# Optimization experiments

Hardware: AMD Instinct MI355X
Metric: run time of the kernel (lower is better)

## Reference

```python
import jax, jax.numpy as jnp
import numpy as np

N_NODES = 50000
N_EDGES = 800000
IN_DIM, HID_DIM, LAT_DIM = 64, 64, 32


def _glorot(key, fan_in, fan_out):
    s = jnp.sqrt(6.0 / (fan_in + fan_out))
    return jax.random.uniform(key, (fan_in, fan_out), jnp.float32, -s, s)


def setup_inputs() -> dict:
    key = jax.random.key(0)
    ks = jax.random.split(key, 8)
    x = jax.random.normal(ks[0], (N_NODES, IN_DIM), jnp.float32)
    edge_index = jax.random.randint(ks[1], (2, N_EDGES), 0, N_NODES, jnp.int64)
    W1 = _glorot(ks[2], IN_DIM, HID_DIM)
    b1 = jnp.zeros((HID_DIM,), jnp.float32)
    W2 = _glorot(ks[3], HID_DIM, HID_DIM)
    b2 = jnp.zeros((HID_DIM,), jnp.float32)
    W3 = _glorot(ks[4], HID_DIM, LAT_DIM)
    b3 = jnp.zeros((LAT_DIM,), jnp.float32)
    return {"x": x, "edge_index": edge_index, "W1": W1, "b1": b1,
            "W2": W2, "b2": b2, "W3": W3, "b3": b3}


def _self_loop_edges(edge_index, n):
    loop = jnp.arange(n, dtype=edge_index.dtype)
    src = jnp.concatenate([edge_index[0], loop])
    dst = jnp.concatenate([edge_index[1], loop])
    return src, dst


def _gcn_norm(src, dst, n):
    # deg over A + I (unit edge weights), computed on target column (PyG default)
    deg = jax.ops.segment_sum(jnp.ones_like(dst, dtype=jnp.float32), dst, num_segments=n)
    dinv = jnp.where(deg > 0, jax.lax.rsqrt(deg), 0.0)
    return dinv[src] * dinv[dst]  # [E+N]


def _gcn_conv(x, src, dst, norm, W, b, n):
    h = x @ W                         # [N, out] small GEMM first, as in PyG
    msg = h[src] * norm[:, None]      # gather + scale, [E+N, out]
    out = jax.ops.segment_sum(msg, dst, num_segments=n)  # scatter-add
    return out + b


def reference(x, edge_index, W1, b1, W2, b2, W3, b3):
    n = x.shape[0]
    src, dst = _self_loop_edges(edge_index, n)
    norm = _gcn_norm(src, dst, n)
    h = jnp.tanh(_gcn_conv(x, src, dst, norm, W1, b1, n))
    h = jnp.tanh(_gcn_conv(h, src, dst, norm, W2, b2, n))
    z = _gcn_conv(h, src, dst, norm, W3, b3, n)
    return z
```

## Files before the change

kernel.cpp:

```cpp
#include <hip/hip_runtime.h>
#include <hip/hip_bf16.h>


#define IN_DIM 64
#define HID_DIM 64
#define LAT_DIM 32
#define BCAP 5120


__global__ __launch_bounds__(256) void bin_kernel(const int* __restrict__ src,
                                                  const int* __restrict__ dst,
                                                  int* __restrict__ bucket_cnt,
                                                  unsigned* __restrict__ pairs, int E) {
    __shared__ int bcnt[256];
    __shared__ int bbase[256];
    int tid = threadIdx.x;
    bcnt[tid] = 0;
    __syncthreads();
    int base = blockIdx.x * 4096;
    unsigned pk[16]; int bk[16]; int rk[16];
    #pragma unroll
    for (int i = 0; i < 16; ++i) {
        int e = base + i * 256 + tid;
        bk[i] = -1;
        if (e < E) {
            int s = __builtin_nontemporal_load(src + e);
            int d = __builtin_nontemporal_load(dst + e);
            bk[i] = d >> 8;
            pk[i] = (unsigned)s | ((unsigned)(d & 255) << 16);
            rk[i] = atomicAdd(&bcnt[bk[i]], 1);
        }
    }
    __syncthreads();
    int c = bcnt[tid];
    if (c > 0) bbase[tid] = atomicAdd(&bucket_cnt[tid], c);
    __syncthreads();
    #pragma unroll
    for (int i = 0; i < 16; ++i) {
        if (bk[i] >= 0) {
            int pos = bbase[bk[i]] + rk[i];
            if (pos < BCAP) pairs[(size_t)bk[i] * BCAP + pos] = pk[i];
        }
    }
}

__global__ __launch_bounds__(256) void bscan_kernel(const int* __restrict__ bucket_cnt,
                                                    int* __restrict__ boff, int NBK) {
    __shared__ int wtot[4];
    int tid = threadIdx.x;
    int lane = tid & 63, wid = tid >> 6;
    int v = (tid < NBK) ? min(bucket_cnt[tid], BCAP) : 0;
    int sc = v;
    #pragma unroll
    for (int d = 1; d < 64; d <<= 1) {
        int t = __shfl_up(sc, d, 64);
        if (lane >= d) sc += t;
    }
    if (lane == 63) wtot[wid] = sc;
    __syncthreads();
    int woff = 0;
    #pragma unroll
    for (int w = 0; w < 4; ++w) if (w < wid) woff += wtot[w];
    boff[tid] = woff + sc - v;
}

__global__ __launch_bounds__(256) void build_off_kernel(const unsigned* __restrict__ pairs,
                                                        const int* __restrict__ bucket_cnt,
                                                        const int* __restrict__ boff,
                                                        int* __restrict__ off,
                                                        float* __restrict__ dinv, int N) {
    __shared__ int h[256];
    __shared__ int wtot[4];
    int b = blockIdx.x, tid = threadIdx.x;
    h[tid] = 0;
    __syncthreads();
    int c = min(bucket_cnt[b], BCAP);
    const unsigned* pb = pairs + (size_t)b * BCAP;
    for (int i = tid; i < c; i += 256)
        atomicAdd(&h[pb[i] >> 16], 1);
    __syncthreads();
    int v = h[tid];
    int lane = tid & 63, wid = tid >> 6;
    int sc = v;
    #pragma unroll
    for (int d = 1; d < 64; d <<= 1) {
        int t = __shfl_up(sc, d, 64);
        if (lane >= d) sc += t;
    }
    if (lane == 63) wtot[wid] = sc;
    __syncthreads();
    int woff = 0;
    #pragma unroll
    for (int w = 0; w < 4; ++w) if (w < wid) woff += wtot[w];
    int incl = woff + sc;
    int node = b * 256 + tid;
    if (node < N) {
        off[node + 1] = boff[b] + incl;
        dinv[node]    = rsqrtf((float)(v + 1));
    }
    if (b == 0 && tid == 0) off[0] = 0;
}

__global__ __launch_bounds__(256) void bscatter_kernel(const unsigned* __restrict__ pairs,
                                                       const int* __restrict__ bucket_cnt,
                                                       const int* __restrict__ off,
                                                       int* __restrict__ col, int N) {
    __shared__ int scur[256];
    int b = blockIdx.x, tid = threadIdx.x;
    int node = b * 256 + tid;
    scur[tid] = (node < N) ? off[node] : 0;
    __syncthreads();
    int c = min(bucket_cnt[b], BCAP);
    const unsigned* pb = pairs + (size_t)b * BCAP;
    for (int i = tid; i < c; i += 256) {
        unsigned v = pb[i];
        int p = atomicAdd(&scur[v >> 16], 1);
        col[p] = (int)(v & 0xFFFFu);
    }
}


template<int OUT, int RT>
__global__ __launch_bounds__(256) void gemm_tile_kernel(const float* __restrict__ X,
                                                        const float* __restrict__ W,
                                                        const float* __restrict__ dinv,
                                                        float* __restrict__ G, int N) {
    constexpr int CG = OUT / 4;
    static_assert(256 / CG * 4 == RT, "RT must match 4*(256/CG)");
    __shared__ float Ws[64 * OUT];
    __shared__ float Xs[RT][64 + 4];
    int tid = threadIdx.x;
    int row0 = blockIdx.x * RT;

    for (int f = 4 * tid; f < 64 * OUT; f += 1024)
        *(float4*)&Ws[f] = *(const float4*)&W[f];

    for (int f = 4 * tid; f < RT * 64; f += 1024) {
        int r  = f >> 6;
        int k0 = f & 63;
        int gr = row0 + r;
        float4 v = (gr < N) ? *(const float4*)&X[(size_t)gr * 64 + k0]
                            : make_float4(0.f, 0.f, 0.f, 0.f);
        *(float4*)&Xs[r][k0] = v;
    }
    __syncthreads();

    int cr = tid % CG;
    int rr = tid / CG;
    float acc[4][4] = {};
    #pragma unroll 4
    for (int k = 0; k < 64; ++k) {
        float4 bv = *(float4*)&Ws[k * OUT + 4 * cr];
        float av[4] = {Xs[4 * rr + 0][k], Xs[4 * rr + 1][k],
                       Xs[4 * rr + 2][k], Xs[4 * rr + 3][k]};
        float bb[4] = {bv.x, bv.y, bv.z, bv.w};
        #pragma unroll
        for (int j = 0; j < 4; ++j)
            #pragma unroll
            for (int i = 0; i < 4; ++i)
                acc[j][i] += av[j] * bb[i];
    }

    #pragma unroll
    for (int j = 0; j < 4; ++j) {
        int gr = row0 + 4 * rr + j;
        if (gr < N) {
            float s = dinv[gr];
            float4 o = make_float4(acc[j][0] * s, acc[j][1] * s,
                                   acc[j][2] * s, acc[j][3] * s);
            *(float4*)&G[(size_t)gr * OUT + 4 * cr] = o;
        }
    }
}


template<int D, bool TANH>
__global__ __launch_bounds__(256) void agg_kernel(const float* __restrict__ G,
                           const int* __restrict__ off,
                           const int* __restrict__ col, const float* __restrict__ dinv,
                           const float* __restrict__ b, float* __restrict__ H, int N) {
    constexpr int F = D / 32;
    int tid  = threadIdx.x;
    int lane = tid & 63;
    int w    = tid >> 6;
    int node = blockIdx.x * 4 + w;
    if (node >= N) return;
    int grp = lane >> 3;
    int c4  = lane & 7;
    int p0  = off[node];
    int total = off[node + 1] - p0 + 1;
    float4 a0 = make_float4(0.f, 0.f, 0.f, 0.f);
    float4 a1 = make_float4(0.f, 0.f, 0.f, 0.f);
    #pragma unroll 2
    for (int base = 0; base < total; base += 8) {
        int e = base + grp;
        if (e < total) {
            int s = (e == 0) ? node : col[p0 + e - 1];
            const float4* row = (const float4*)&G[(size_t)s * D];
            float4 u = row[c4];
            a0.x += u.x; a0.y += u.y; a0.z += u.z; a0.w += u.w;
            if (F == 2) {
                float4 u2 = row[c4 + 8];
                a1.x += u2.x; a1.y += u2.y; a1.z += u2.z; a1.w += u2.w;
            }
        }
    }
    #pragma unroll
    for (int m = 8; m < 64; m <<= 1) {
        a0.x += __shfl_xor(a0.x, m, 64);
        a0.y += __shfl_xor(a0.y, m, 64);
        a0.z += __shfl_xor(a0.z, m, 64);
        a0.w += __shfl_xor(a0.w, m, 64);
        if (F == 2) {
            a1.x += __shfl_xor(a1.x, m, 64);
            a1.y += __shfl_xor(a1.y, m, 64);
            a1.z += __shfl_xor(a1.z, m, 64);
            a1.w += __shfl_xor(a1.w, m, 64);
        }
    }
    if (grp == 0) {
        float s = dinv[node];
        float4 bq = *(const float4*)&b[4 * c4];
        float4 o;
        o.x = s * a0.x + bq.x; o.y = s * a0.y + bq.y;
        o.z = s * a0.z + bq.z; o.w = s * a0.w + bq.w;
        if (TANH) { o.x = tanhf(o.x); o.y = tanhf(o.y); o.z = tanhf(o.z); o.w = tanhf(o.w); }
        *(float4*)&H[(size_t)node * D + 4 * c4] = o;
        if (F == 2) {
            float4 bq1 = *(const float4*)&b[4 * (c4 + 8)];
            float4 o1;
            o1.x = s * a1.x + bq1.x; o1.y = s * a1.y + bq1.y;
            o1.z = s * a1.z + bq1.z; o1.w = s * a1.w + bq1.w;
            if (TANH) { o1.x = tanhf(o1.x); o1.y = tanhf(o1.y);
                        o1.z = tanhf(o1.z); o1.w = tanhf(o1.w); }
            *(float4*)&H[(size_t)node * D + 4 * (c4 + 8)] = o1;
        }
    }
}


static inline size_t align256(size_t x) { return (x + 255) & ~(size_t)255; }

extern "C" void kernel_launch(void* const* d_in, const int* in_sizes, int n_in,
                              void* d_out, int out_size, void* d_ws, size_t ws_size,
                              hipStream_t stream) {
    const float* x   = (const float*)d_in[0];
    const int*   ei  = (const int*)d_in[1];
    const float* W1  = (const float*)d_in[2];
    const float* b1  = (const float*)d_in[3];
    const float* W2  = (const float*)d_in[4];
    const float* b2  = (const float*)d_in[5];
    const float* W3  = (const float*)d_in[6];
    const float* b3  = (const float*)d_in[7];
    float* out = (float*)d_out;

    const int N = in_sizes[0] / IN_DIM;
    const int E = in_sizes[1] / 2;
    const int* src = ei;
    const int* dst = ei + E;
    const int NBK  = (N + 255) / 256;
    const int BINB = (E + 4095) / 4096;

    char* ws = (char*)d_ws;
    size_t o = 0;
    int*      bkcnt = (int*)(ws + o);      o = align256(o + 256 * 4);
    int*      boff  = (int*)(ws + o);      o = align256(o + 256 * 4);
    int*      off   = (int*)(ws + o);      o = align256(o + (size_t)(N + 1) * 4);
    float*    dinv  = (float*)(ws + o);    o = align256(o + (size_t)N * 4);
    unsigned* pairs = (unsigned*)(ws + o); o = align256(o + (size_t)NBK * BCAP * 4);
    int*      col   = (int*)(ws + o);      o = align256(o + (size_t)E * 4);
    float*    bufG  = (float*)(ws + o);    o = align256(o + (size_t)N * HID_DIM * 4);
    float*    bufH  = (float*)(ws + o);    o = align256(o + (size_t)N * HID_DIM * 4);
    (void)ws_size;

    hipMemsetAsync(bkcnt, 0, 256 * 4, stream);
    bin_kernel<<<BINB, 256, 0, stream>>>(src, dst, bkcnt, pairs, E);
    bscan_kernel<<<1, 256, 0, stream>>>(bkcnt, boff, NBK);
    build_off_kernel<<<NBK, 256, 0, stream>>>(pairs, bkcnt, boff, off, dinv, N);

    const int g64_grid = (N + 63) / 64;
    const int g32_grid = (N + 127) / 128;
    const int agg_grid = (N + 3) / 4;

    gemm_tile_kernel<HID_DIM, 64><<<g64_grid, 256, 0, stream>>>(x, W1, dinv, bufG, N);
    bscatter_kernel<<<NBK, 256, 0, stream>>>(pairs, bkcnt, off, col, N);

    agg_kernel<HID_DIM, true><<<agg_grid, 256, 0, stream>>>(bufG, off, col, dinv, b1, bufH, N);
    gemm_tile_kernel<HID_DIM, 64><<<g64_grid, 256, 0, stream>>>(bufH, W2, dinv, bufG, N);
    agg_kernel<HID_DIM, true><<<agg_grid, 256, 0, stream>>>(bufG, off, col, dinv, b2, bufH, N);
    gemm_tile_kernel<LAT_DIM, 128><<<g32_grid, 256, 0, stream>>>(bufH, W3, dinv, bufG, N);
    agg_kernel<LAT_DIM, false><<<agg_grid, 256, 0, stream>>>(bufG, off, col, dinv, b3, out, N);
}
```

Before: 238.6 us.

## Store intermediate features in fp16 and fuse CSR build kernels

Intermediate G and H buffers are now stored as fp16, which halves the bytes moved by the gather-heavy aggregation and GEMM loads. Accumulation still happens in fp32. The aggregation kernel is reworked to read half8 chunks. Separately, the bucket scan, offset build and column scatter are merged into one kernel, with each block recomputing the bucket prefix itself, so two launches go away. The cost is fp16 rounding of activations, which could affect output accuracy.

```diff
diff --git a/kernel.cpp b/kernel.cpp
--- a/kernel.cpp
+++ b/kernel.cpp
@@ -1,11 +1,15 @@
 #include <hip/hip_runtime.h>
-#include <hip/hip_bf16.h>
+#include <hip/hip_fp16.h>
+#include <type_traits>
 
 
 #define IN_DIM 64
 #define HID_DIM 64
 #define LAT_DIM 32
 #define BCAP 5120
+
+typedef __attribute__((ext_vector_type(8))) _Float16 half8;
+typedef __attribute__((ext_vector_type(4))) _Float16 half4;
 
 
 __global__ __launch_bounds__(256) void bin_kernel(const int* __restrict__ src,
@@ -44,11 +48,19 @@
     }
 }
 
-__global__ __launch_bounds__(256) void bscan_kernel(const int* __restrict__ bucket_cnt,
-                                                    int* __restrict__ boff, int NBK) {
+__global__ __launch_bounds__(256) void build_csr_kernel(const unsigned* __restrict__ pairs,
+                                                        const int* __restrict__ bucket_cnt,
+                                                        int* __restrict__ off,
+                                                        float* __restrict__ dinv,
+                                                        int* __restrict__ col,
+                                                        int N, int NBK) {
+    __shared__ int sboff[256];
+    __shared__ int h[256];
+    __shared__ int scur[256];
     __shared__ int wtot[4];
-    int tid = threadIdx.x;
+    int b = blockIdx.x, tid = threadIdx.x;
     int lane = tid & 63, wid = tid >> 6;
+
     int v = (tid < NBK) ? min(bucket_cnt[tid], BCAP) : 0;
     int sc = v;
     #pragma unroll
@@ -57,74 +69,56 @@
         if (lane >= d) sc += t;
     }
     if (lane == 63) wtot[wid] = sc;
+    h[tid] = 0;
     __syncthreads();
     int woff = 0;
     #pragma unroll
     for (int w = 0; w < 4; ++w) if (w < wid) woff += wtot[w];
-    boff[tid] = woff + sc - v;
-}
-
-__global__ __launch_bounds__(256) void build_off_kernel(const unsigned* __restrict__ pairs,
-                                                        const int* __restrict__ bucket_cnt,
-                                                        const int* __restrict__ boff,
-                                                        int* __restrict__ off,
-                                                        float* __restrict__ dinv, int N) {
-    __shared__ int h[256];
-    __shared__ int wtot[4];
-    int b = blockIdx.x, tid = threadIdx.x;
-    h[tid] = 0;
-    __syncthreads();
+    sboff[tid] = woff + sc - v;
+    __syncthreads();
+    int boff_b = sboff[b];
+
     int c = min(bucket_cnt[b], BCAP);
     const unsigned* pb = pairs + (size_t)b * BCAP;
     for (int i = tid; i < c; i += 256)
         atomicAdd(&h[pb[i] >> 16], 1);
     __syncthreads();
-    int v = h[tid];
-    int lane = tid & 63, wid = tid >> 6;
-    int sc = v;
+
+    int hv = h[tid];
+    int sc2 = hv;
     #pragma unroll
     for (int d = 1; d < 64; d <<= 1) {
-        int t = __shfl_up(sc, d, 64);
-        if (lane >= d) sc += t;
-    }
-    if (lane == 63) wtot[wid] = sc;
-    __syncthreads();
-    int woff = 0;
-    #pragma unroll
-    for (int w = 0; w < 4; ++w) if (w < wid) woff += wtot[w];
-    int incl = woff + sc;
+        int t = __shfl_up(sc2, d, 64);
+        if (lane >= d) sc2 += t;
+    }
+    if (lane == 63) wtot[wid] = sc2;
+    __syncthreads();
+    int woff2 = 0;
+    #pragma unroll
+    for (int w = 0; w < 4; ++w) if (w < wid) woff2 += wtot[w];
+    int incl = woff2 + sc2;
     int node = b * 256 + tid;
+    scur[tid] = boff_b + incl - hv;
     if (node < N) {
-        off[node + 1] = boff[b] + incl;
-        dinv[node]    = rsqrtf((float)(v + 1));
+        off[node + 1] = boff_b + incl;
+        dinv[node]    = rsqrtf((float)(hv + 1));
     }
     if (b == 0 && tid == 0) off[0] = 0;
-}
-
-__global__ __launch_bounds__(256) void bscatter_kernel(const unsigned* __restrict__ pairs,
-                                                       const int* __restrict__ bucket_cnt,
-                                                       const int* __restrict__ off,
-                                                       int* __restrict__ col, int N) {
-    __shared__ int scur[256];
-    int b = blockIdx.x, tid = threadIdx.x;
-    int node = b * 256 + tid;
-    scur[tid] = (node < N) ? off[node] : 0;
-    __syncthreads();
-    int c = min(bucket_cnt[b], BCAP);
-    const unsigned* pb = pairs + (size_t)b * BCAP;
+    __syncthreads();
+
     for (int i = tid; i < c; i += 256) {
-        unsigned v = pb[i];
-        int p = atomicAdd(&scur[v >> 16], 1);
-        col[p] = (int)(v & 0xFFFFu);
-    }
-}
-
-
-template<int OUT, int RT>
-__global__ __launch_bounds__(256) void gemm_tile_kernel(const float* __restrict__ X,
+        unsigned p = pb[i];
+        int pos = atomicAdd(&scur[p >> 16], 1);
+        col[pos] = (int)(p & 0xFFFFu);
+    }
+}
+
+
+template<int OUT, int RT, typename TIN>
+__global__ __launch_bounds__(256) void gemm_tile_kernel(const TIN* __restrict__ X,
                                                         const float* __restrict__ W,
                                                         const float* __restrict__ dinv,
-                                                        float* __restrict__ G, int N) {
+                                                        _Float16* __restrict__ G, int N) {
     constexpr int CG = OUT / 4;
     static_assert(256 / CG * 4 == RT, "RT must match 4*(256/CG)");
     __shared__ float Ws[64 * OUT];
@@ -135,13 +129,25 @@
     for (int f = 4 * tid; f < 64 * OUT; f += 1024)
         *(float4*)&Ws[f] = *(const float4*)&W[f];
 
-    for (int f = 4 * tid; f < RT * 64; f += 1024) {
-        int r  = f >> 6;
-        int k0 = f & 63;
-        int gr = row0 + r;
-        float4 v = (gr < N) ? *(const float4*)&X[(size_t)gr * 64 + k0]
-                            : make_float4(0.f, 0.f, 0.f, 0.f);
-        *(float4*)&Xs[r][k0] = v;
+    if constexpr (std::is_same<TIN, float>::value) {
+        for (int f = 4 * tid; f < RT * 64; f += 1024) {
+            int r = f >> 6, k0 = f & 63, gr = row0 + r;
+            float4 v = (gr < N) ? *(const float4*)&X[(size_t)gr * 64 + k0]
+                                : make_float4(0.f, 0.f, 0.f, 0.f);
+            *(float4*)&Xs[r][k0] = v;
+        }
+    } else {
+        for (int f = 8 * tid; f < RT * 64; f += 2048) {
+            int r = f >> 6, k0 = f & 63, gr = row0 + r;
+            if (gr < N) {
+                half8 v = *(const half8*)&X[(size_t)gr * 64 + k0];
+                #pragma unroll
+                for (int i = 0; i < 8; ++i) Xs[r][k0 + i] = (float)v[i];
+            } else {
+                #pragma unroll
+                for (int i = 0; i < 8; ++i) Xs[r][k0 + i] = 0.f;
+            }
+        }
     }
     __syncthreads();
 
@@ -166,74 +172,65 @@
         int gr = row0 + 4 * rr + j;
         if (gr < N) {
             float s = dinv[gr];
-            float4 o = make_float4(acc[j][0] * s, acc[j][1] * s,
-                                   acc[j][2] * s, acc[j][3] * s);
-            *(float4*)&G[(size_t)gr * OUT + 4 * cr] = o;
-        }
-    }
-}
-
-
-template<int D, bool TANH>
-__global__ __launch_bounds__(256) void agg_kernel(const float* __restrict__ G,
+            half4 o;
+            #pragma unroll
+            for (int i = 0; i < 4; ++i) o[i] = (_Float16)(acc[j][i] * s);
+            *(half4*)&G[(size_t)gr * OUT + 4 * cr] = o;
+        }
+    }
+}
+
+
+template<int D, bool TANH, typename TOUT>
+__global__ __launch_bounds__(256) void agg_kernel(const _Float16* __restrict__ G,
                            const int* __restrict__ off,
                            const int* __restrict__ col, const float* __restrict__ dinv,
-                           const float* __restrict__ b, float* __restrict__ H, int N) {
-    constexpr int F = D / 32;
+                           const float* __restrict__ b, TOUT* __restrict__ H, int N) {
+    constexpr int CHUNKS = D / 8;
+    constexpr int EPI = 64 / CHUNKS;
     int tid  = threadIdx.x;
     int lane = tid & 63;
     int w    = tid >> 6;
     int node = blockIdx.x * 4 + w;
     if (node >= N) return;
-    int grp = lane >> 3;
-    int c4  = lane & 7;
+    int grp = lane / CHUNKS;
+    int c4  = lane % CHUNKS;
     int p0  = off[node];
     int total = off[node + 1] - p0 + 1;
-    float4 a0 = make_float4(0.f, 0.f, 0.f, 0.f);
-    float4 a1 = make_float4(0.f, 0.f, 0.f, 0.f);
+    float acc[8] = {};
     #pragma unroll 2
-    for (int base = 0; base < total; base += 8) {
+    for (int base = 0; base < total; base += EPI) {
         int e = base + grp;
         if (e < total) {
             int s = (e == 0) ? node : col[p0 + e - 1];
-            const float4* row = (const float4*)&G[(size_t)s * D];
-            float4 u = row[c4];
-            a0.x += u.x; a0.y += u.y; a0.z += u.z; a0.w += u.w;
-            if (F == 2) {
-                float4 u2 = row[c4 + 8];
-                a1.x += u2.x; a1.y += u2.y; a1.z += u2.z; a1.w += u2.w;
-            }
-        }
-    }
-    #pragma unroll
-    for (int m = 8; m < 64; m <<= 1) {
-        a0.x += __shfl_xor(a0.x, m, 64);
-        a0.y += __shfl_xor(a0.y, m, 64);
-        a0.z += __shfl_xor(a0.z, m, 64);
-        a0.w += __shfl_xor(a0.w, m, 64);
-        if (F == 2) {
-            a1.x += __shfl_xor(a1.x, m, 64);
-            a1.y += __shfl_xor(a1.y, m, 64);
-            a1.z += __shfl_xor(a1.z, m, 64);
-            a1.w += __shfl_xor(a1.w, m, 64);
-        }
+            half8 u = *(const half8*)&G[(size_t)s * D + 8 * c4];
+            #pragma unroll
+            for (int i = 0; i < 8; ++i) acc[i] += (float)u[i];
+        }
+    }
+    #pragma unroll
+    for (int m = CHUNKS; m < 64; m <<= 1) {
+        #pragma unroll
+        for (int i = 0; i < 8; ++i) acc[i] += __shfl_xor(acc[i], m, 64);
     }
     if (grp == 0) {
         float s = dinv[node];
-        float4 bq = *(const float4*)&b[4 * c4];
-        float4 o;
-        o.x = s * a0.x + bq.x; o.y = s * a0.y + bq.y;
-        o.z = s * a0.z + bq.z; o.w = s * a0.w + bq.w;
-        if (TANH) { o.x = tanhf(o.x); o.y = tanhf(o.y); o.z = tanhf(o.z); o.w = tanhf(o.w); }
-        *(float4*)&H[(size_t)node * D + 4 * c4] = o;
-        if (F == 2) {
-            float4 bq1 = *(const float4*)&b[4 * (c4 + 8)];
-            float4 o1;
-            o1.x = s * a1.x + bq1.x; o1.y = s * a1.y + bq1.y;
-            o1.z = s * a1.z + bq1.z; o1.w = s * a1.w + bq1.w;
-            if (TANH) { o1.x = tanhf(o1.x); o1.y = tanhf(o1.y);
-                        o1.z = tanhf(o1.z); o1.w = tanhf(o1.w); }
-            *(float4*)&H[(size_t)node * D + 4 * (c4 + 8)] = o1;
+        float o[8];
+        #pragma unroll
+        for (int i = 0; i < 8; ++i) {
+            o[i] = s * acc[i] + b[8 * c4 + i];
+            if (TANH) o[i] = tanhf(o[i]);
+        }
+        if constexpr (std::is_same<TOUT, _Float16>::value) {
+            half8 hv;
+            #pragma unroll
+            for (int i = 0; i < 8; ++i) hv[i] = (_Float16)o[i];
+            *(half8*)&H[(size_t)node * D + 8 * c4] = hv;
+        } else {
+            float4 f0 = make_float4(o[0], o[1], o[2], o[3]);
+            float4 f1 = make_float4(o[4], o[5], o[6], o[7]);
+            *(float4*)&H[(size_t)node * D + 8 * c4 + 0] = f0;
+            *(float4*)&H[(size_t)node * D + 8 * c4 + 4] = f1;
         }
     }
 }
@@ -263,31 +260,27 @@
 
     char* ws = (char*)d_ws;
     size_t o = 0;
-    int*      bkcnt = (int*)(ws + o);      o = align256(o + 256 * 4);
-    int*      boff  = (int*)(ws + o);      o = align256(o + 256 * 4);
-    int*      off   = (int*)(ws + o);      o = align256(o + (size_t)(N + 1) * 4);
-    float*    dinv  = (float*)(ws + o);    o = align256(o + (size_t)N * 4);
-    unsigned* pairs = (unsigned*)(ws + o); o = align256(o + (size_t)NBK * BCAP * 4);
-    int*      col   = (int*)(ws + o);      o = align256(o + (size_t)E * 4);
-    float*    bufG  = (float*)(ws + o);    o = align256(o + (size_t)N * HID_DIM * 4);
-    float*    bufH  = (float*)(ws + o);    o = align256(o + (size_t)N * HID_DIM * 4);
+    int*       bkcnt = (int*)(ws + o);       o = align256(o + 256 * 4);
+    int*       off   = (int*)(ws + o);       o = align256(o + (size_t)(N + 1) * 4);
+    float*     dinv  = (float*)(ws + o);     o = align256(o + (size_t)N * 4);
+    unsigned*  pairs = (unsigned*)(ws + o);  o = align256(o + (size_t)NBK * BCAP * 4);
+    int*       col   = (int*)(ws + o);       o = align256(o + (size_t)E * 4);
+    _Float16*  bufG  = (_Float16*)(ws + o);  o = align256(o + (size_t)N * HID_DIM * 2);
+    _Float16*  bufH  = (_Float16*)(ws + o);  o = align256(o + (size_t)N * HID_DIM * 2);
     (void)ws_size;
 
     hipMemsetAsync(bkcnt, 0, 256 * 4, stream);
     bin_kernel<<<BINB, 256, 0, stream>>>(src, dst, bkcnt, pairs, E);
-    bscan_kernel<<<1, 256, 0, stream>>>(bkcnt, boff, NBK);
-    build_off_kernel<<<NBK, 256, 0, stream>>>(pairs, bkcnt, boff, off, dinv, N);
+    build_csr_kernel<<<NBK, 256, 0, stream>>>(pairs, bkcnt, off, dinv, col, N, NBK);
 
     const int g64_grid = (N + 63) / 64;
     const int g32_grid = (N + 127) / 128;
     const int agg_grid = (N + 3) / 4;
 
-    gemm_tile_kernel<HID_DIM, 64><<<g64_grid, 256, 0, stream>>>(x, W1, dinv, bufG, N);
-    bscatter_kernel<<<NBK, 256, 0, stream>>>(pairs, bkcnt, off, col, N);
-
-    agg_kernel<HID_DIM, true><<<agg_grid, 256, 0, stream>>>(bufG, off, col, dinv, b1, bufH, N);
-    gemm_tile_kernel<HID_DIM, 64><<<g64_grid, 256, 0, stream>>>(bufH, W2, dinv, bufG, N);
-    agg_kernel<HID_DIM, true><<<agg_grid, 256, 0, stream>>>(bufG, off, col, dinv, b2, bufH, N);
-    gemm_tile_kernel<LAT_DIM, 128><<<g32_grid, 256, 0, stream>>>(bufH, W3, dinv, bufG, N);
-    agg_kernel<LAT_DIM, false><<<agg_grid, 256, 0, stream>>>(bufG, off, col, dinv, b3, out, N);
-}
+    gemm_tile_kernel<HID_DIM, 64, float><<<g64_grid, 256, 0, stream>>>(x, W1, dinv, bufG, N);
+    agg_kernel<HID_DIM, true, _Float16><<<agg_grid, 256, 0, stream>>>(bufG, off, col, dinv, b1, bufH, N);
+    gemm_tile_kernel<HID_DIM, 64, _Float16><<<g64_grid, 256, 0, stream>>>(bufH, W2, dinv, bufG, N);
+    agg_kernel<HID_DIM, true, _Float16><<<agg_grid, 256, 0, stream>>>(bufG, off, col, dinv, b2, bufH, N);
+    gemm_tile_kernel<LAT_DIM, 128, _Float16><<<g32_grid, 256, 0, stream>>>(bufH, W3, dinv, bufG, N);
+    agg_kernel<LAT_DIM, false, float><<<agg_grid, 256, 0, stream>>>(bufG, off, col, dinv, b3, out, N);
+}
```

After: 236.3 us. Within noise of the previous version (-1.0%).
